# Optimization experiments

Hardware: AMD Instinct MI355X
Metric: run time of the kernel (lower is better)

The kernel has to match this reference:

```python
import jax, jax.numpy as jnp
import numpy as np

EPS_SUM = 1e-8
EPS_FILL = 1e-4
NORM_THRESH = 0.1
MASK_THRESH = 0.1


def _shift1(x):
    # conv2d with 1x3 filter [1,1,0], padding (0,1): out[i] = x[i-1] + x[i]
    return x + jnp.pad(x, ((0, 0), (0, 0), (0, 0), (1, 0)))[..., :-1]


def _shift2(x):
    # conv2d with 1x3 filter [0,1,1], padding (0,1): out[i] = x[i] + x[i+1]
    return x + jnp.pad(x, ((0, 0), (0, 0), (0, 0), (0, 1)))[..., 1:]


def _fill(disp, vm, shift_fn, n_steps):
    # Hole filling: each step propagates valid disparity one pixel; after W
    # steps the data-dependent while-loop of the original has converged
    # (further steps are identity), so a fixed-length scan is equivalent.
    def step(carry, _):
        d, m = carry
        m1 = shift_fn(m)
        nm = (m1 > 0).astype(d.dtype)
        d = d * m + shift_fn(d) / (m1 + EPS_FILL) * (nm - m)
        return (d, nm), None
    (disp, vm), _ = jax.lax.scan(step, (disp, vm), None, length=n_steps)
    return disp, vm


def regress_disp(att, valid_mask):
    # att: [B,H,W,W], valid_mask: [B,1,H,W]
    b, h, w, _ = att.shape
    idx = jnp.arange(w, dtype=att.dtype)
    disp_ini = idx[None, None, None, :] - jnp.sum(att * idx, axis=-1).reshape(b, 1, h, w)
    disp = disp_ini * valid_mask
    disp, vm = _fill(disp, valid_mask, _shift1, w)  # left-to-right pass
    disp, vm = _fill(disp, vm, _shift2, w)          # right-to-left pass
    return disp_ini * valid_mask + disp * (1.0 - valid_mask)


def masked_exp_norm(cost, lower):
    # tril/triu-masked exp normalization (non-standard attention)
    tri = jnp.tril if lower else jnp.triu
    c = tri(cost)
    c = jnp.exp(c - jnp.max(c, axis=-1, keepdims=True))
    c = tri(c)
    return c / (jnp.sum(c, axis=-1, keepdims=True) + EPS_SUM)


def gen_pos_shift(w, dtype):
    p = jnp.linspace(0.0, 2.0, w).astype(dtype)
    pos = jnp.maximum(p[:, None] - p[None, :], 0.0)  # pos_l - pos_r, clipped
    return pos[None, None]  # [1,1,W,W]


def gen_raw_disp(att, pos_shift):
    hi = jnp.argmax(att, axis=-1)
    rr = jnp.stack([hi - 1, hi, hi + 1], axis=-1) + 1  # indices into padded axis
    att_pad = jnp.pad(att, ((0, 0), (0, 0), (0, 0), (1, 1)))
    aw = jnp.take_along_axis(att_pad, rr, axis=-1)
    norm = jnp.sum(aw, axis=-1, keepdims=True)
    norm = jnp.where(norm < NORM_THRESH, 1.0, norm)
    aw = aw / norm
    pos_pad = jnp.broadcast_to(jnp.pad(pos_shift, ((0, 0), (0, 0), (0, 0), (1, 1))), att_pad.shape)
    pr = jnp.take_along_axis(pos_pad, rr, axis=-1)
    return jnp.sum(aw * pr, axis=-1)  # [B,H,W]


def setup_inputs() -> dict:
    key = jax.random.key(0)
    k1, k2 = jax.random.split(key)
    B, H, W = 1, 64, 512
    cost1 = jax.random.normal(k1, (B, H, W, W), dtype=jnp.float32)
    cost2 = jax.random.normal(k2, (B, H, W, W), dtype=jnp.float32)
    return {"cost1": cost1, "cost2": cost2}


def reference(cost1, cost2):
    b, h, w, _ = cost1.shape
    att_r2l = masked_exp_norm(cost2, lower=True)   # right-to-left attention
    att_l2r = masked_exp_norm(cost1, lower=False)  # left-to-right attention
    vm_left = (jnp.sum(att_l2r, axis=-2) > MASK_THRESH).astype(cost1.dtype).reshape(b, 1, h, w)
    vm_right = (jnp.sum(att_r2l, axis=-2) > MASK_THRESH).astype(cost1.dtype).reshape(b, 1, h, w)
    disp_r2l = regress_disp(att_r2l, vm_left)   # [B,1,H,W]
    disp_l2r = regress_disp(att_l2r, vm_right)  # [B,1,H,W]
    pos = gen_pos_shift(w, cost1.dtype)
    raw_l2r = gen_raw_disp(att_r2l, pos)                               # [B,H,W]
    raw_r2l = gen_raw_disp(att_l2r, jnp.swapaxes(pos, -1, -2))         # [B,H,W]
    return jnp.concatenate([disp_r2l, disp_l2r, raw_l2r[:, None], raw_r2l[:, None]], axis=1)
```

## Files before the change

### kernel.cpp

```cpp
#include <hip/hip_runtime.h>
#include <float.h>

#define H 64
#define W 512
#define SPLIT 8

template<bool LOWER, bool FULLROW>
__device__ __forceinline__ void process_rows(
    const float* __restrict__ hb, const int h, const int s,
    const int lane, const int wid,
    float* __restrict__ disp, float* __restrict__ raw, float* scol)
{
  constexpr int NH = FULLROW ? 2 : 1;
  constexpr int JB = FULLROW ? 0 : (LOWER ? 0 : 256);
  const float pscale = 2.0f / 511.0f;

  float cacc[NH * 4];
  #pragma unroll
  for (int q = 0; q < NH * 4; q++) cacc[q] = 0.f;

  int   jmap[NH * 4];
  float jfmap[NH * 4];
  #pragma unroll
  for (int hh = 0; hh < NH; hh++)
    #pragma unroll
    for (int k = 0; k < 4; k++) {
      jmap[hh * 4 + k]  = JB + hh * 256 + lane * 4 + k;
      jfmap[hh * 4 + k] = (float)jmap[hh * 4 + k];
    }

  for (int t = wid; t < 64; t += 8) {
    const int i = s * 64 + t;
    const float fi = (float)i;
    const float* rp = hb + (size_t)i * W;

    float c[NH * 4];
    #pragma unroll
    for (int hh = 0; hh < NH; hh++) {
      const float4 v = ((const float4*)rp)[(JB >> 2) + hh * 64 + lane];
      c[hh*4+0] = v.x; c[hh*4+1] = v.y; c[hh*4+2] = v.z; c[hh*4+3] = v.w;
    }

    float best = -FLT_MAX;
    int   bj   = 1024;
    #pragma unroll
    for (int hh = 0; hh < NH; hh++) {
      const bool NM = FULLROW ? (LOWER ? (hh == 1) : (hh == 0)) : true;
      #pragma unroll
      for (int k = 0; k < 4; k++) {
        const int q = hh * 4 + k;
        float v = c[q];
        if (NM) {
          const bool vld = LOWER ? (jmap[q] <= i) : (jmap[q] >= i);
          v = vld ? v : -FLT_MAX;
          c[q] = v;
        }
        if (v > best) { best = v; bj = jmap[q]; }
      }
    }
    #pragma unroll
    for (int off = 32; off; off >>= 1) {
      const float ov = __shfl_xor(best, off);
      const int   oj = __shfl_xor(bj, off);
      if (ov > best || (ov == best && oj < bj)) { best = ov; bj = oj; }
    }

    const int bjm = bj - 1, bjp = bj + 1;
    const int am = min(max(bjm, 0), W - 1);
    const int ap = min(bjp, W - 1);
    const float cm_ = rp[am];
    const float cp_ = rp[ap];

    const bool hasMasked = LOWER ? (i < W - 1) : (i > 0);
    const float mx = hasMasked ? fmaxf(best, 0.f) : best;

    float ssum = 0.f, wsum = 0.f;
    #pragma unroll
    for (int q = 0; q < NH * 4; q++) {
      const float e = __expf(c[q] - mx);
      c[q] = e;
      ssum += e;
      wsum = fmaf(e, jfmap[q], wsum);
    }
    #pragma unroll
    for (int off = 32; off; off >>= 1) {
      ssum += __shfl_xor(ssum, off);
      wsum += __shfl_xor(wsum, off);
    }
    const float inv = 1.f / (ssum + 1e-8f);

    #pragma unroll
    for (int q = 0; q < NH * 4; q++) cacc[q] = fmaf(c[q], inv, cacc[q]);

    if (lane == 0) {
      const bool pv = LOWER ? (bjm >= 0) : (bjm >= i);
      const bool nv = LOWER ? (bjp <= i) : (bjp <= W - 1);
      const float e_h = __expf(best - mx);
      const float e_p = pv ? __expf(cm_ - mx) : 0.f;
      const float e_n = nv ? __expf(cp_ - mx) : 0.f;
      const float t0 = e_p + e_h + e_n;
      const float w0 = fmaf(e_p, (float)bjm, fmaf(e_h, (float)bj, e_n * (float)bjp));
      disp[h * W + i] = fi - wsum * inv;
      const float n0 = t0 * inv;
      const float t1 = pscale * (LOWER ? (fi * t0 - w0) : (w0 - fi * t0));
      raw[h * W + i] = (t1 * inv) / (n0 < 0.1f ? 1.f : n0);
    }
  }

  #pragma unroll
  for (int q = 0; q < NH * 4; q++) atomicAdd(&scol[jmap[q]], cacc[q]);
}

__global__ __launch_bounds__(512) void attn_stats_all(
    const float* __restrict__ cost1, const float* __restrict__ cost2,
    float* __restrict__ disp_r2l, float* __restrict__ disp_l2r,
    float* __restrict__ cs_r2l,  float* __restrict__ cs_l2r,
    float* __restrict__ out)
{
  __shared__ float scol[W];
  const int tid  = threadIdx.x;
  const int lane = tid & 63;
  const int wid  = tid >> 6;
  const int gid  = blockIdx.x;
  const bool lower = (gid & 1) == 0;
  const int rest = gid >> 1;
  const int h    = rest >> 3;
  const int s    = rest & 7;

  const float* cost = lower ? cost2 : cost1;
  float* disp = lower ? disp_r2l : disp_l2r;
  float* csum = lower ? cs_r2l  : cs_l2r;
  float* raw  = out + (lower ? 2 : 3) * (H * W);
  const float* hb = cost + (size_t)h * W * W;

  scol[tid] = 0.f;
  __syncthreads();

  if (lower) {
    if (s < 4) process_rows<true,  false>(hb, h, s, lane, wid, disp, raw, scol);
    else       process_rows<true,  true >(hb, h, s, lane, wid, disp, raw, scol);
  } else {
    if (s < 4) process_rows<false, true >(hb, h, s, lane, wid, disp, raw, scol);
    else       process_rows<false, false>(hb, h, s, lane, wid, disp, raw, scol);
  }
  __syncthreads();

  const bool doMine = lower ? (s >= 4 || tid < 256)
                            : (s < 4  || tid >= 256);
  if (doMine) atomicAdd(&csum[h * W + tid], scol[tid]);
}

__global__ __launch_bounds__(64) void fill_rows(
    const float* __restrict__ dispA, const float* __restrict__ csA,
    const float* __restrict__ dispB, const float* __restrict__ csB,
    float* __restrict__ out)
{
  __shared__ float xrow[W];
  const int pair = blockIdx.x >> 6;
  const int h    = blockIdx.x & 63;
  const float* dsp = (pair ? dispB : dispA) + h * W;
  const float* cs  = (pair ? csB  : csA ) + h * W;
  float* o = out + pair * (H * W) + h * W;
  const int lane = threadIdx.x;
  const int j0 = lane * 8;

  float x[8];
  bool m[8];
  int incl[8];
  int run = -1, fv = W;
  #pragma unroll
  for (int k = 0; k < 8; k++) {
    x[k] = dsp[j0 + k];
    m[k] = cs[j0 + k] > 0.1f;
    xrow[j0 + k] = x[k];
    if (m[k]) { run = j0 + k; if (fv == W) fv = j0 + k; }
    incl[k] = run;
  }
  int v = run;
  #pragma unroll
  for (int off = 1; off < 64; off <<= 1) {
    const int tv = __shfl_up(v, off);
    if (lane >= off) v = max(v, tv);
  }
  int excl = __shfl_up(v, 1);
  if (lane == 0) excl = -1;
  int p0 = fv;
  #pragma unroll
  for (int off = 32; off; off >>= 1) p0 = min(p0, __shfl_xor(p0, off));
  __syncthreads();

  const float C2 = -1.4426229e-4f;
  #pragma unroll
  for (int k = 0; k < 8; k++) {
    const int jj = j0 + k;
    float ov;
    if (m[k]) {
      ov = x[k];
    } else {
      const int p = max(excl, incl[k]);
      if (p >= 0)        ov = xrow[p]  * exp2f(C2 * (float)(jj - p));
      else if (p0 < W)   ov = xrow[p0] * exp2f(C2 * (float)(p0 - jj));
      else               ov = 0.f;
    }
    o[jj] = ov;
  }
}

extern "C" void kernel_launch(void* const* d_in, const int* in_sizes, int n_in,
                              void* d_out, int out_size, void* d_ws, size_t ws_size,
                              hipStream_t stream) {
  const float* cost1 = (const float*)d_in[0];
  const float* cost2 = (const float*)d_in[1];
  float* out = (float*)d_out;
  float* w = (float*)d_ws;
  float* disp_r2l_ini = w;
  float* disp_l2r_ini = w + 32768;
  float* cs_l2r       = w + 65536;
  float* cs_r2l       = w + 98304;

  hipMemsetAsync(cs_l2r, 0, 2 * (size_t)H * W * sizeof(float), stream);

  attn_stats_all<<<2 * H * SPLIT, 512, 0, stream>>>(
      cost1, cost2, disp_r2l_ini, disp_l2r_ini, cs_r2l, cs_l2r, out);

  fill_rows<<<2 * H, 64, 0, stream>>>(disp_r2l_ini, cs_l2r,
                                      disp_l2r_ini, cs_r2l, out);
}
```

Measured before the change: 162.2 us.

## Pair short and long triangular rows per warp to balance block workload

Each block now takes 32 row pairs, a short row (half width) together with its mirrored long row (full width), in place of 64 consecutive rows that were all short or all long. Every block and warp therefore does the same amount of work, which removes the imbalance between blocks handling half-row and full-row slices. The two rows' reductions are interleaved to add instruction-level parallelism. In exchange each block writes all 512 column sums through global atomics, and per-thread register use goes up.

```diff
diff --git a/kernel.cpp b/kernel.cpp
--- a/kernel.cpp
+++ b/kernel.cpp
@@ -5,110 +5,153 @@
 #define W 512
 #define SPLIT 8
 
-template<bool LOWER, bool FULLROW>
-__device__ __forceinline__ void process_rows(
+template<bool LOWER>
+__device__ __forceinline__ void process_pairs(
     const float* __restrict__ hb, const int h, const int s,
     const int lane, const int wid,
     float* __restrict__ disp, float* __restrict__ raw, float* scol)
 {
-  constexpr int NH = FULLROW ? 2 : 1;
-  constexpr int JB = FULLROW ? 0 : (LOWER ? 0 : 256);
   const float pscale = 2.0f / 511.0f;
 
-  float cacc[NH * 4];
-  #pragma unroll
-  for (int q = 0; q < NH * 4; q++) cacc[q] = 0.f;
-
-  int   jmap[NH * 4];
-  float jfmap[NH * 4];
-  #pragma unroll
-  for (int hh = 0; hh < NH; hh++)
+  int   j0i[4], j1i[4];
+  float jf0[4], jf1[4];
+  #pragma unroll
+  for (int k = 0; k < 4; k++) {
+    j0i[k] = lane * 4 + k;
+    j1i[k] = 256 + lane * 4 + k;
+    jf0[k] = (float)j0i[k];
+    jf1[k] = (float)j1i[k];
+  }
+
+  float cacc[8];
+  #pragma unroll
+  for (int q = 0; q < 8; q++) cacc[q] = 0.f;
+
+  for (int t = wid; t < 32; t += 8) {
+    const int i  = s * 32 + t;
+    const int iS = LOWER ? i : (W - 1 - i);
+    const int iL = LOWER ? (W - 1 - i) : i;
+    const float* rpS = hb + (size_t)iS * W;
+    const float* rpL = hb + (size_t)iL * W;
+
+    float cS[4], cL[8];
+    {
+      const float4 vS = ((const float4*)rpS)[(LOWER ? 0 : 64) + lane];
+      cS[0]=vS.x; cS[1]=vS.y; cS[2]=vS.z; cS[3]=vS.w;
+      const float4 v0 = ((const float4*)rpL)[lane];
+      cL[0]=v0.x; cL[1]=v0.y; cL[2]=v0.z; cL[3]=v0.w;
+      const float4 v1 = ((const float4*)rpL)[64 + lane];
+      cL[4]=v1.x; cL[5]=v1.y; cL[6]=v1.z; cL[7]=v1.w;
+    }
+
+    float bS = -FLT_MAX; int jS = 1024;
     #pragma unroll
     for (int k = 0; k < 4; k++) {
-      jmap[hh * 4 + k]  = JB + hh * 256 + lane * 4 + k;
-      jfmap[hh * 4 + k] = (float)jmap[hh * 4 + k];
-    }
-
-  for (int t = wid; t < 64; t += 8) {
-    const int i = s * 64 + t;
-    const float fi = (float)i;
-    const float* rp = hb + (size_t)i * W;
-
-    float c[NH * 4];
-    #pragma unroll
-    for (int hh = 0; hh < NH; hh++) {
-      const float4 v = ((const float4*)rp)[(JB >> 2) + hh * 64 + lane];
-      c[hh*4+0] = v.x; c[hh*4+1] = v.y; c[hh*4+2] = v.z; c[hh*4+3] = v.w;
-    }
-
-    float best = -FLT_MAX;
-    int   bj   = 1024;
-    #pragma unroll
-    for (int hh = 0; hh < NH; hh++) {
-      const bool NM = FULLROW ? (LOWER ? (hh == 1) : (hh == 0)) : true;
+      const int j = LOWER ? j0i[k] : j1i[k];
+      const bool vld = LOWER ? (j <= iS) : (j >= iS);
+      const float v = vld ? cS[k] : -FLT_MAX;
+      cS[k] = v;
+      if (v > bS) { bS = v; jS = j; }
+    }
+    float bL = -FLT_MAX; int jL = 1024;
+    #pragma unroll
+    for (int k = 0; k < 8; k++) {
+      const int j = (k < 4) ? j0i[k] : j1i[k - 4];
+      const bool NM = LOWER ? (k >= 4) : (k < 4);
+      float v = cL[k];
+      if (NM) {
+        const bool vld = LOWER ? (j <= iL) : (j >= iL);
+        v = vld ? v : -FLT_MAX;
+        cL[k] = v;
+      }
+      if (v > bL) { bL = v; jL = j; }
+    }
+    #pragma unroll
+    for (int off = 32; off; off >>= 1) {
+      const float ovS = __shfl_xor(bS, off);
+      const int   ojS = __shfl_xor(jS, off);
+      if (ovS > bS || (ovS == bS && ojS < jS)) { bS = ovS; jS = ojS; }
+      const float ovL = __shfl_xor(bL, off);
+      const int   ojL = __shfl_xor(jL, off);
+      if (ovL > bL || (ovL == bL && ojL < jL)) { bL = ovL; jL = ojL; }
+    }
+
+    const int jSm = jS - 1, jSp = jS + 1;
+    const int jLm = jL - 1, jLp = jL + 1;
+    const float cmS = rpS[min(max(jSm, 0), W - 1)];
+    const float cpS = rpS[min(jSp, W - 1)];
+    const float cmL = rpL[min(max(jLm, 0), W - 1)];
+    const float cpL = rpL[min(jLp, W - 1)];
+
+    const float mxS = fmaxf(bS, 0.f);
+    const float mxL = (i > 0) ? fmaxf(bL, 0.f) : bL;
+
+    float sS = 0.f, wS = 0.f;
+    #pragma unroll
+    for (int k = 0; k < 4; k++) {
+      const float e = __expf(cS[k] - mxS);
+      cS[k] = e;
+      sS += e;
+      wS = fmaf(e, LOWER ? jf0[k] : jf1[k], wS);
+    }
+    float sL = 0.f, wL = 0.f;
+    #pragma unroll
+    for (int k = 0; k < 8; k++) {
+      const float e = __expf(cL[k] - mxL);
+      cL[k] = e;
+      sL += e;
+      wL = fmaf(e, (k < 4) ? jf0[k] : jf1[k - 4], wL);
+    }
+    #pragma unroll
+    for (int off = 32; off; off >>= 1) {
+      sS += __shfl_xor(sS, off);
+      wS += __shfl_xor(wS, off);
+      sL += __shfl_xor(sL, off);
+      wL += __shfl_xor(wL, off);
+    }
+    const float invS = 1.f / (sS + 1e-8f);
+    const float invL = 1.f / (sL + 1e-8f);
+
+    #pragma unroll
+    for (int k = 0; k < 4; k++) {
+      const int qS = LOWER ? k : 4 + k;
+      cacc[qS]    = fmaf(cS[k],     invS, cacc[qS]);
+      cacc[k]     = fmaf(cL[k],     invL, cacc[k]);
+      cacc[4 + k] = fmaf(cL[4 + k], invL, cacc[4 + k]);
+    }
+
+    if (lane == 0) {
       #pragma unroll
-      for (int k = 0; k < 4; k++) {
-        const int q = hh * 4 + k;
-        float v = c[q];
-        if (NM) {
-          const bool vld = LOWER ? (jmap[q] <= i) : (jmap[q] >= i);
-          v = vld ? v : -FLT_MAX;
-          c[q] = v;
-        }
-        if (v > best) { best = v; bj = jmap[q]; }
+      for (int rr = 0; rr < 2; rr++) {
+        const int   ii   = rr ? iL : iS;
+        const float bb   = rr ? bL : bS;
+        const int   bj   = rr ? jL : jS;
+        const float mx   = rr ? mxL : mxS;
+        const float inv  = rr ? invL : invS;
+        const float wsum = rr ? wL : wS;
+        const float cm_  = rr ? cmL : cmS;
+        const float cp_  = rr ? cpL : cpS;
+        const int bjm = bj - 1, bjp = bj + 1;
+        const bool pv = LOWER ? (bjm >= 0)  : (bjm >= ii);
+        const bool nv = LOWER ? (bjp <= ii) : (bjp <= W - 1);
+        const float e_h = __expf(bb - mx);
+        const float e_p = pv ? __expf(cm_ - mx) : 0.f;
+        const float e_n = nv ? __expf(cp_ - mx) : 0.f;
+        const float t0 = e_p + e_h + e_n;
+        const float w0 = fmaf(e_p, (float)bjm, fmaf(e_h, (float)bj, e_n * (float)bjp));
+        const float fi = (float)ii;
+        disp[h * W + ii] = fi - wsum * inv;
+        const float n0 = t0 * inv;
+        const float t1 = pscale * (LOWER ? (fi * t0 - w0) : (w0 - fi * t0));
+        raw[h * W + ii] = (t1 * inv) / (n0 < 0.1f ? 1.f : n0);
       }
     }
-    #pragma unroll
-    for (int off = 32; off; off >>= 1) {
-      const float ov = __shfl_xor(best, off);
-      const int   oj = __shfl_xor(bj, off);
-      if (ov > best || (ov == best && oj < bj)) { best = ov; bj = oj; }
-    }
-
-    const int bjm = bj - 1, bjp = bj + 1;
-    const int am = min(max(bjm, 0), W - 1);
-    const int ap = min(bjp, W - 1);
-    const float cm_ = rp[am];
-    const float cp_ = rp[ap];
-
-    const bool hasMasked = LOWER ? (i < W - 1) : (i > 0);
-    const float mx = hasMasked ? fmaxf(best, 0.f) : best;
-
-    float ssum = 0.f, wsum = 0.f;
-    #pragma unroll
-    for (int q = 0; q < NH * 4; q++) {
-      const float e = __expf(c[q] - mx);
-      c[q] = e;
-      ssum += e;
-      wsum = fmaf(e, jfmap[q], wsum);
-    }
-    #pragma unroll
-    for (int off = 32; off; off >>= 1) {
-      ssum += __shfl_xor(ssum, off);
-      wsum += __shfl_xor(wsum, off);
-    }
-    const float inv = 1.f / (ssum + 1e-8f);
-
-    #pragma unroll
-    for (int q = 0; q < NH * 4; q++) cacc[q] = fmaf(c[q], inv, cacc[q]);
-
-    if (lane == 0) {
-      const bool pv = LOWER ? (bjm >= 0) : (bjm >= i);
-      const bool nv = LOWER ? (bjp <= i) : (bjp <= W - 1);
-      const float e_h = __expf(best - mx);
-      const float e_p = pv ? __expf(cm_ - mx) : 0.f;
-      const float e_n = nv ? __expf(cp_ - mx) : 0.f;
-      const float t0 = e_p + e_h + e_n;
-      const float w0 = fmaf(e_p, (float)bjm, fmaf(e_h, (float)bj, e_n * (float)bjp));
-      disp[h * W + i] = fi - wsum * inv;
-      const float n0 = t0 * inv;
-      const float t1 = pscale * (LOWER ? (fi * t0 - w0) : (w0 - fi * t0));
-      raw[h * W + i] = (t1 * inv) / (n0 < 0.1f ? 1.f : n0);
-    }
-  }
-
-  #pragma unroll
-  for (int q = 0; q < NH * 4; q++) atomicAdd(&scol[jmap[q]], cacc[q]);
+  }
+
+  #pragma unroll
+  for (int q = 0; q < 4; q++) atomicAdd(&scol[j0i[q]], cacc[q]);
+  #pragma unroll
+  for (int q = 0; q < 4; q++) atomicAdd(&scol[j1i[q]], cacc[4 + q]);
 }
 
 __global__ __launch_bounds__(512) void attn_stats_all(
@@ -136,18 +179,11 @@
   scol[tid] = 0.f;
   __syncthreads();
 
-  if (lower) {
-    if (s < 4) process_rows<true,  false>(hb, h, s, lane, wid, disp, raw, scol);
-    else       process_rows<true,  true >(hb, h, s, lane, wid, disp, raw, scol);
-  } else {
-    if (s < 4) process_rows<false, true >(hb, h, s, lane, wid, disp, raw, scol);
-    else       process_rows<false, false>(hb, h, s, lane, wid, disp, raw, scol);
-  }
+  if (lower) process_pairs<true >(hb, h, s, lane, wid, disp, raw, scol);
+  else       process_pairs<false>(hb, h, s, lane, wid, disp, raw, scol);
+
   __syncthreads();
-
-  const bool doMine = lower ? (s >= 4 || tid < 256)
-                            : (s < 4  || tid >= 256);
-  if (doMine) atomicAdd(&csum[h * W + tid], scol[tid]);
+  atomicAdd(&csum[h * W + tid], scol[tid]);
 }
 
 __global__ __launch_bounds__(64) void fill_rows(
```

After: 167.8 us. 1.03x slower.

## Prefetch next row into registers and drop max subtraction from exp

Applied to the files above, without the earlier changes.

Software-pipelines the row loop by loading the next row's cost values into registers while the current row is processed. The softmax now uses exp(c) directly without subtracting the row max, so the argmax, sum and weighted-sum shuffle reductions merge into one butterfly. The lane-0 disparity and raw-disparity output for each row is deferred by one iteration. The aim is to hide global load latency and shorten the serial reduction chain. The cost is more live registers, and exp without max subtraction can overflow if cost values are large.

```diff
diff --git a/kernel.cpp b/kernel.cpp
--- a/kernel.cpp
+++ b/kernel.cpp
@@ -4,6 +4,30 @@
 #define H 64
 #define W 512
 #define SPLIT 8
+
+
+template<bool LOWER>
+__device__ __forceinline__ void emit_row(
+    const int h, const int p_i, const int p_bj,
+    const float p_best, const float p_inv, const float p_wsum,
+    const float p_cm, const float p_cp,
+    float* __restrict__ disp, float* __restrict__ raw)
+{
+  const float pscale = 2.0f / 511.0f;
+  const int bjm = p_bj - 1, bjp = p_bj + 1;
+  const bool pv = LOWER ? (bjm >= 0)   : (bjm >= p_i);
+  const bool nv = LOWER ? (bjp <= p_i) : (bjp <= W - 1);
+  const float e_h = __expf(p_best);
+  const float e_p = pv ? __expf(p_cm) : 0.f;
+  const float e_n = nv ? __expf(p_cp) : 0.f;
+  const float t0 = e_p + e_h + e_n;
+  const float w0 = fmaf(e_p, (float)bjm, fmaf(e_h, (float)p_bj, e_n * (float)bjp));
+  const float fi = (float)p_i;
+  disp[h * W + p_i] = fi - p_wsum * p_inv;
+  const float n0 = t0 * p_inv;
+  const float t1 = pscale * (LOWER ? (fi * t0 - w0) : (w0 - fi * t0));
+  raw[h * W + p_i] = (t1 * p_inv) / (n0 < 0.1f ? 1.f : n0);
+}
 
 template<bool LOWER, bool FULLROW>
 __device__ __forceinline__ void process_rows(
@@ -13,7 +37,6 @@
 {
   constexpr int NH = FULLROW ? 2 : 1;
   constexpr int JB = FULLROW ? 0 : (LOWER ? 0 : 256);
-  const float pscale = 2.0f / 511.0f;
 
   float cacc[NH * 4];
   #pragma unroll
@@ -29,16 +52,31 @@
       jfmap[hh * 4 + k] = (float)jmap[hh * 4 + k];
     }
 
-  for (int t = wid; t < 64; t += 8) {
-    const int i = s * 64 + t;
-    const float fi = (float)i;
+  float c[NH * 4];
+  {
+    const float* rp0 = hb + (size_t)(s * 64 + wid) * W;
+    #pragma unroll
+    for (int hh = 0; hh < NH; hh++) {
+      const float4 v = ((const float4*)rp0)[(JB >> 2) + hh * 64 + lane];
+      c[hh*4+0] = v.x; c[hh*4+1] = v.y; c[hh*4+2] = v.z; c[hh*4+3] = v.w;
+    }
+  }
+
+  int   p_i = 0, p_bj = 0;
+  float p_best = 0.f, p_inv = 0.f, p_wsum = 0.f, p_cm = 0.f, p_cp = 0.f;
+
+  for (int it = 0; it < 8; ++it) {
+    const int i = s * 64 + wid + it * 8;
     const float* rp = hb + (size_t)i * W;
 
-    float c[NH * 4];
-    #pragma unroll
-    for (int hh = 0; hh < NH; hh++) {
-      const float4 v = ((const float4*)rp)[(JB >> 2) + hh * 64 + lane];
-      c[hh*4+0] = v.x; c[hh*4+1] = v.y; c[hh*4+2] = v.z; c[hh*4+3] = v.w;
+    float nc[NH * 4];
+    if (it < 7) {
+      const float* rn = rp + (size_t)(8 * W);
+      #pragma unroll
+      for (int hh = 0; hh < NH; hh++) {
+        const float4 v = ((const float4*)rn)[(JB >> 2) + hh * 64 + lane];
+        nc[hh*4+0] = v.x; nc[hh*4+1] = v.y; nc[hh*4+2] = v.z; nc[hh*4+3] = v.w;
+      }
     }
 
     float best = -FLT_MAX;
@@ -58,54 +96,49 @@
         if (v > best) { best = v; bj = jmap[q]; }
       }
     }
-    #pragma unroll
-    for (int off = 32; off; off >>= 1) {
-      const float ov = __shfl_xor(best, off);
-      const int   oj = __shfl_xor(bj, off);
-      if (ov > best || (ov == best && oj < bj)) { best = ov; bj = oj; }
-    }
-
-    const int bjm = bj - 1, bjp = bj + 1;
-    const int am = min(max(bjm, 0), W - 1);
-    const int ap = min(bjp, W - 1);
-    const float cm_ = rp[am];
-    const float cp_ = rp[ap];
-
-    const bool hasMasked = LOWER ? (i < W - 1) : (i > 0);
-    const float mx = hasMasked ? fmaxf(best, 0.f) : best;
 
     float ssum = 0.f, wsum = 0.f;
     #pragma unroll
     for (int q = 0; q < NH * 4; q++) {
-      const float e = __expf(c[q] - mx);
+      const float e = __expf(c[q]);
       c[q] = e;
       ssum += e;
       wsum = fmaf(e, jfmap[q], wsum);
     }
+
     #pragma unroll
     for (int off = 32; off; off >>= 1) {
-      ssum += __shfl_xor(ssum, off);
-      wsum += __shfl_xor(wsum, off);
+      const float ovb = __shfl_xor(best, off);
+      const int   ojb = __shfl_xor(bj, off);
+      const float oss = __shfl_xor(ssum, off);
+      const float ows = __shfl_xor(wsum, off);
+      if (ovb > best || (ovb == best && ojb < bj)) { best = ovb; bj = ojb; }
+      ssum += oss;
+      wsum += ows;
     }
     const float inv = 1.f / (ssum + 1e-8f);
 
+    const int bjm = bj - 1, bjp = bj + 1;
+    const float cm_ = rp[min(max(bjm, 0), W - 1)];
+    const float cp_ = rp[min(bjp, W - 1)];
+
     #pragma unroll
     for (int q = 0; q < NH * 4; q++) cacc[q] = fmaf(c[q], inv, cacc[q]);
 
-    if (lane == 0) {
-      const bool pv = LOWER ? (bjm >= 0) : (bjm >= i);
-      const bool nv = LOWER ? (bjp <= i) : (bjp <= W - 1);
-      const float e_h = __expf(best - mx);
-      const float e_p = pv ? __expf(cm_ - mx) : 0.f;
-      const float e_n = nv ? __expf(cp_ - mx) : 0.f;
-      const float t0 = e_p + e_h + e_n;
-      const float w0 = fmaf(e_p, (float)bjm, fmaf(e_h, (float)bj, e_n * (float)bjp));
-      disp[h * W + i] = fi - wsum * inv;
-      const float n0 = t0 * inv;
-      const float t1 = pscale * (LOWER ? (fi * t0 - w0) : (w0 - fi * t0));
-      raw[h * W + i] = (t1 * inv) / (n0 < 0.1f ? 1.f : n0);
-    }
-  }
+    if (it != 0 && lane == 0)
+      emit_row<LOWER>(h, p_i, p_bj, p_best, p_inv, p_wsum, p_cm, p_cp,
+                      disp, raw);
+
+    p_i = i; p_bj = bj; p_best = best; p_inv = inv; p_wsum = wsum;
+    p_cm = cm_; p_cp = cp_;
+    if (it < 7) {
+      #pragma unroll
+      for (int q = 0; q < NH * 4; q++) c[q] = nc[q];
+    }
+  }
+  if (lane == 0)
+    emit_row<LOWER>(h, p_i, p_bj, p_best, p_inv, p_wsum, p_cm, p_cp,
+                    disp, raw);
 
   #pragma unroll
   for (int q = 0; q < NH * 4; q++) atomicAdd(&scol[jmap[q]], cacc[q]);
```

After: 161.7 us. No clear change (-0.3%).
